# Kernel optimization log

Hardware: AMD Instinct MI355X
Metric: run time of the kernel (lower is better)

## Reference

```python
import jax, jax.numpy as jnp
import numpy as np

B, S, E = 8192, 7, 2048


def _convolute(X, kernel):
    # X: (B, L, E), kernel: (h, E) -> (B, L-h+1, E)
    # y[b, j] = sum_i X[b, j+i] * kernel[i]  (depthwise sliding-window MAC)
    h = kernel.shape[0]
    L = X.shape[1] - h + 1
    y = X[:, 0:L] * kernel[0]
    for i in range(1, h):
        y = y + X[:, i:i + L] * kernel[i]
    return y


def setup_inputs() -> dict:
    key = jax.random.key(0)
    ks = jax.random.split(key, 5)
    return {
        "X": jax.random.normal(ks[0], (B, S, E), dtype=jnp.float32),
        "conv1": jax.random.normal(ks[1], (2, E), dtype=jnp.float32),
        "conv2": jax.random.normal(ks[2], (2, E), dtype=jnp.float32),
        "conv3": jax.random.normal(ks[3], (3, E), dtype=jnp.float32),
        "conv4": jax.random.normal(ks[4], (3, E), dtype=jnp.float32),
    }


def reference(X, conv1, conv2, conv3, conv4):
    # sentence_size == 7 path: 7 -> 6 -> 5 -> 3 -> 1
    X = jnp.tanh(_convolute(X, conv1))
    X = jnp.tanh(_convolute(X, conv2))
    X = jnp.tanh(_convolute(X, conv3))
    X = jnp.tanh(_convolute(X, conv4))
    return X.reshape(X.shape[0], -1)  # (B, E)
```

## Files before the change

kernel.cpp:

```cpp
#include <hip/hip_runtime.h>

#define BB 8192
#define SS 7
#define EE 2048
#define EV (EE / 4)
#define BPT 8

typedef float v4f __attribute__((ext_vector_type(4)));

__device__ __forceinline__ float fast_tanh(float x) {
    float e = exp2f(x * 2.885390081777927f);
    return fmaf(-2.f, __builtin_amdgcn_rcpf(e + 1.f), 1.f);
}

__global__ __launch_bounds__(256, 4) void CSM_62216896250027_kernel(
    const v4f* __restrict__ Xv,
    const v4f* __restrict__ c1,
    const v4f* __restrict__ c2,
    const v4f* __restrict__ c3,
    const v4f* __restrict__ c4,
    v4f* __restrict__ out)
{
    const int t  = blockIdx.x * blockDim.x + threadIdx.x;
    const int ev = t & (EV - 1);
    const int bt = t >> 9;
    const int b0 = bt * BPT;

    v4f k1[2], k2[2], k3[3], k4[3];
    #pragma unroll
    for (int i = 0; i < 2; ++i) {
        k1[i] = c1[i * EV + ev];
        k2[i] = c2[i * EV + ev];
    }
    #pragma unroll
    for (int i = 0; i < 3; ++i) {
        k3[i] = c3[i * EV + ev];
        k4[i] = c4[i * EV + ev];
    }

    const v4f* xp = Xv + (size_t)b0 * SS * EV + ev;
    v4f*       op = out + (size_t)b0 * EV + ev;

    #pragma unroll 2
    for (int i = 0; i < BPT; ++i) {
        v4f xx[SS];
        #pragma unroll
        for (int s = 0; s < SS; ++s)
            xx[s] = __builtin_nontemporal_load(xp + s * EV);

        v4f r;
        #pragma unroll
        for (int j = 0; j < 4; ++j) {
            float y1[6];
            #pragma unroll
            for (int s = 0; s < 6; ++s)
                y1[s] = fast_tanh(fmaf(xx[s][j], k1[0][j], xx[s + 1][j] * k1[1][j]));
            float y2[5];
            #pragma unroll
            for (int s = 0; s < 5; ++s)
                y2[s] = fast_tanh(fmaf(y1[s], k2[0][j], y1[s + 1] * k2[1][j]));
            float y3[3];
            #pragma unroll
            for (int s = 0; s < 3; ++s)
                y3[s] = fast_tanh(fmaf(y2[s], k3[0][j],
                                  fmaf(y2[s + 1], k3[1][j], y2[s + 2] * k3[2][j])));
            r[j] = fast_tanh(fmaf(y3[0], k4[0][j],
                             fmaf(y3[1], k4[1][j], y3[2] * k4[2][j])));
        }

        __builtin_nontemporal_store(r, op);
        xp += SS * EV;
        op += EV;
    }
}

extern "C" void kernel_launch(void* const* d_in, const int* in_sizes, int n_in,
                              void* d_out, int out_size, void* d_ws, size_t ws_size,
                              hipStream_t stream) {
    const v4f* X  = (const v4f*)d_in[0];
    const v4f* c1 = (const v4f*)d_in[1];
    const v4f* c2 = (const v4f*)d_in[2];
    const v4f* c3 = (const v4f*)d_in[3];
    const v4f* c4 = (const v4f*)d_in[4];
    v4f* out = (v4f*)d_out;

    const int total_threads = EV * (BB / BPT);
    const int block = 256;
    const int grid  = total_threads / block;
    CSM_62216896250027_kernel<<<grid, block, 0, stream>>>(X, c1, c2, c3, c4, out);
}
```

Baseline: 111.7 us.

## Use float2 lanes, prefetch next batch row, fold tanh scale into weights

Each thread now handles two embedding channels instead of four, which doubles the thread count. It prefetches the next batch's seven input vectors into registers while computing the current one, with the loop fully unrolled. The tanh pre-scale constant is multiplied into the conv weights once, so each activation saves a multiply, and the math uses packed v2f operations that may map to packed FMA. Launch bounds rise to 6 waves per SIMD. Together these aim to hide memory latency and cut ALU work, at the cost of narrower 8-byte loads and more register pressure from the double buffer.

```diff
diff --git a/kernel.cpp b/kernel.cpp
--- a/kernel.cpp
+++ b/kernel.cpp
@@ -3,88 +3,100 @@
 #define BB 8192
 #define SS 7
 #define EE 2048
-#define EV (EE / 4)
+#define EV2 (EE / 2)
 #define BPT 8
 
-typedef float v4f __attribute__((ext_vector_type(4)));
+typedef float v2f __attribute__((ext_vector_type(2)));
 
-__device__ __forceinline__ float fast_tanh(float x) {
-    float e = exp2f(x * 2.885390081777927f);
-    return fmaf(-2.f, __builtin_amdgcn_rcpf(e + 1.f), 1.f);
+#define SC 2.885390081777927f
+
+__device__ __forceinline__ v2f tanh2(v2f s) {
+    v2f e, r;
+    e.x = exp2f(s.x);
+    e.y = exp2f(s.y);
+    v2f d = e + 1.0f;
+    r.x = __builtin_amdgcn_rcpf(d.x);
+    r.y = __builtin_amdgcn_rcpf(d.y);
+    return 1.0f - 2.0f * r;
 }
 
-__global__ __launch_bounds__(256, 4) void CSM_62216896250027_kernel(
-    const v4f* __restrict__ Xv,
-    const v4f* __restrict__ c1,
-    const v4f* __restrict__ c2,
-    const v4f* __restrict__ c3,
-    const v4f* __restrict__ c4,
-    v4f* __restrict__ out)
+__global__ __launch_bounds__(256, 6) void CSM_62216896250027_kernel(
+    const v2f* __restrict__ Xv,
+    const v2f* __restrict__ c1,
+    const v2f* __restrict__ c2,
+    const v2f* __restrict__ c3,
+    const v2f* __restrict__ c4,
+    v2f* __restrict__ out)
 {
-    const int t  = blockIdx.x * blockDim.x + threadIdx.x;
-    const int ev = t & (EV - 1);
-    const int bt = t >> 9;
-    const int b0 = bt * BPT;
+    const int t   = blockIdx.x * blockDim.x + threadIdx.x;
+    const int ev  = t & (EV2 - 1);
+    const int bt  = t >> 10;
+    const int b0  = bt * BPT;
 
-    v4f k1[2], k2[2], k3[3], k4[3];
+    v2f k1[2], k2[2], k3[3], k4[3];
     #pragma unroll
     for (int i = 0; i < 2; ++i) {
-        k1[i] = c1[i * EV + ev];
-        k2[i] = c2[i * EV + ev];
+        k1[i] = c1[i * EV2 + ev] * SC;
+        k2[i] = c2[i * EV2 + ev] * SC;
     }
     #pragma unroll
     for (int i = 0; i < 3; ++i) {
-        k3[i] = c3[i * EV + ev];
-        k4[i] = c4[i * EV + ev];
+        k3[i] = c3[i * EV2 + ev] * SC;
+        k4[i] = c4[i * EV2 + ev] * SC;
     }
 
-    const v4f* xp = Xv + (size_t)b0 * SS * EV + ev;
-    v4f*       op = out + (size_t)b0 * EV + ev;
+    const v2f* xp = Xv + (size_t)b0 * SS * EV2 + ev;
+    v2f*       op = out + (size_t)b0 * EV2 + ev;
 
-    #pragma unroll 2
+    v2f xx[SS], xn[SS];
+    #pragma unroll
+    for (int s = 0; s < SS; ++s)
+        xx[s] = __builtin_nontemporal_load(xp + s * EV2);
+    xp += SS * EV2;
+
+    #pragma unroll
     for (int i = 0; i < BPT; ++i) {
-        v4f xx[SS];
+        if (i + 1 < BPT) {
+            #pragma unroll
+            for (int s = 0; s < SS; ++s)
+                xn[s] = __builtin_nontemporal_load(xp + s * EV2);
+            xp += SS * EV2;
+        }
+
+        v2f y1[6];
+        #pragma unroll
+        for (int s = 0; s < 6; ++s)
+            y1[s] = tanh2(xx[s] * k1[0] + xx[s + 1] * k1[1]);
+        v2f y2[5];
+        #pragma unroll
+        for (int s = 0; s < 5; ++s)
+            y2[s] = tanh2(y1[s] * k2[0] + y1[s + 1] * k2[1]);
+        v2f y3[3];
+        #pragma unroll
+        for (int s = 0; s < 3; ++s)
+            y3[s] = tanh2(y2[s] * k3[0] + y2[s + 1] * k3[1] + y2[s + 2] * k3[2]);
+        v2f y4 = tanh2(y3[0] * k4[0] + y3[1] * k4[1] + y3[2] * k4[2]);
+
+        __builtin_nontemporal_store(y4, op);
+        op += EV2;
+
         #pragma unroll
         for (int s = 0; s < SS; ++s)
-            xx[s] = __builtin_nontemporal_load(xp + s * EV);
-
-        v4f r;
-        #pragma unroll
-        for (int j = 0; j < 4; ++j) {
-            float y1[6];
-            #pragma unroll
-            for (int s = 0; s < 6; ++s)
-                y1[s] = fast_tanh(fmaf(xx[s][j], k1[0][j], xx[s + 1][j] * k1[1][j]));
-            float y2[5];
-            #pragma unroll
-            for (int s = 0; s < 5; ++s)
-                y2[s] = fast_tanh(fmaf(y1[s], k2[0][j], y1[s + 1] * k2[1][j]));
-            float y3[3];
-            #pragma unroll
-            for (int s = 0; s < 3; ++s)
-                y3[s] = fast_tanh(fmaf(y2[s], k3[0][j],
-                                  fmaf(y2[s + 1], k3[1][j], y2[s + 2] * k3[2][j])));
-            r[j] = fast_tanh(fmaf(y3[0], k4[0][j],
-                             fmaf(y3[1], k4[1][j], y3[2] * k4[2][j])));
-        }
-
-        __builtin_nontemporal_store(r, op);
-        xp += SS * EV;
-        op += EV;
+            xx[s] = xn[s];
     }
 }
 
 extern "C" void kernel_launch(void* const* d_in, const int* in_sizes, int n_in,
                               void* d_out, int out_size, void* d_ws, size_t ws_size,
                               hipStream_t stream) {
-    const v4f* X  = (const v4f*)d_in[0];
-    const v4f* c1 = (const v4f*)d_in[1];
-    const v4f* c2 = (const v4f*)d_in[2];
-    const v4f* c3 = (const v4f*)d_in[3];
-    const v4f* c4 = (const v4f*)d_in[4];
-    v4f* out = (v4f*)d_out;
+    const v2f* X  = (const v2f*)d_in[0];
+    const v2f* c1 = (const v2f*)d_in[1];
+    const v2f* c2 = (const v2f*)d_in[2];
+    const v2f* c3 = (const v2f*)d_in[3];
+    const v2f* c4 = (const v2f*)d_in[4];
+    v2f* out = (v2f*)d_out;
 
-    const int total_threads = EV * (BB / BPT);
+    const int total_threads = EV2 * (BB / BPT);
     const int block = 256;
     const int grid  = total_threads / block;
     CSM_62216896250027_kernel<<<grid, block, 0, stream>>>(X, c1, c2, c3, c4, out);
```

Result: faster. 106.9 us (-4.3%).
